# Kernel tuning notes

Hardware: AMD Instinct MI355X
Metric: run time of the kernel (lower is better)

Reference implementation:

```python
import jax, jax.numpy as jnp
import numpy as np

EPS = 1e-12  # torch F.normalize eps

def _l2norm(v, axis):
    n = jnp.linalg.norm(v, axis=axis, keepdims=True)
    return v / jnp.maximum(n, EPS)

def setup_inputs() -> dict:
    key = jax.random.key(0)
    k1, k2, k3 = jax.random.split(key, 3)
    N, D, H, W, K = 32, 512, 40, 40, 64
    x = jax.random.normal(k1, (N, D, H, W), dtype=jnp.float32)
    conv_weight = jax.random.normal(k2, (K, D), dtype=jnp.float32) * 0.05
    centroids = jax.random.uniform(k3, (K, D), dtype=jnp.float32)
    return {"x": x, "conv_weight": conv_weight, "centroids": centroids}

def reference(x, conv_weight, centroids):
    N, D, H, W = x.shape
    K = centroids.shape[0]
    # descriptor-wise L2 normalization over channel dim
    x = _l2norm(x, axis=1)
    x_flat = x.reshape(N, D, H * W)                       # [N, D, S]
    # 1x1 conv == per-pixel linear: [K,D] @ [N,D,S] -> [N,K,S]
    logits = jnp.einsum('kd,nds->nks', conv_weight, x_flat)
    soft_assign = jax.nn.softmax(logits, axis=1)          # softmax over clusters
    # vlad[n,k,d] = sum_s a[n,k,s] * (x[n,d,s] - c[k,d])
    #            = (a @ x^T) - (sum_s a) * c   -- two GEMM-like ops, no K-loop
    agg = jnp.einsum('nks,nds->nkd', soft_assign, x_flat)  # [N, K, D]
    a_sum = soft_assign.sum(axis=2)                        # [N, K]
    vlad = agg - a_sum[:, :, None] * centroids[None, :, :]
    # intra-normalization over D, flatten, global L2 normalization
    vlad = _l2norm(vlad, axis=2)
    vlad = vlad.reshape(N, K * D)
    vlad = _l2norm(vlad, axis=1)
    return vlad
```

## Files before the change

kernel.cpp:

```cpp
#include <hip/hip_runtime.h>
#include <math.h>

#define N_ 32
#define D_ 512
#define S_ 1600
#define K_ 64

typedef __attribute__((ext_vector_type(8))) short short8;
typedef __attribute__((ext_vector_type(4))) float f32x4;

static __device__ __forceinline__ short f2bf(float f) {
    unsigned u = __float_as_uint(f);
    u += 0x7fffu + ((u >> 16) & 1u);
    return (short)(u >> 16);
}

__global__ __launch_bounds__(256) void kW(const float* __restrict__ w,
                                          short* __restrict__ w16)
{
    int i4 = (blockIdx.x * 256 + threadIdx.x) * 4;
    float4 v = *(const float4*)&w[i4];
    short4 h = {f2bf(v.x), f2bf(v.y), f2bf(v.z), f2bf(v.w)};
    *(short4*)&w16[i4] = h;
}

#define TP 72

__global__ __launch_bounds__(256) void kA(const float* __restrict__ x,
                                          const short* __restrict__ w16,
                                          short* __restrict__ aprime,
                                          float* __restrict__ asum)
{
    __shared__ short T[64 * TP];
    __shared__ float pssq[16 * 66];
    __shared__ float invL[64];
    __shared__ float wred[2][4][64];

    const int tid = threadIdx.x;
    const int n  = blockIdx.x / 25;
    const int s0 = (blockIdx.x % 25) * 64;
    const int wv = tid >> 6;
    const int l  = tid & 63;
    const int lk = l & 15;
    const int q  = l >> 4;

    const float* xb = x + (size_t)n * D_ * S_ + s0;
    const int sg = (tid & 15) * 4;
    const int dg = tid >> 4;

    f32x4 acc[4];
#pragma unroll
    for (int st = 0; st < 4; ++st) acc[st] = (f32x4){0.f, 0.f, 0.f, 0.f};
    float ssql[4] = {0.f, 0.f, 0.f, 0.f};

    for (int dc = 0; dc < D_; dc += 64) {
        __syncthreads();
#pragma unroll
        for (int j = 0; j < 4; ++j) {
            int dci = dg + 16 * j;
            float4 v = *(const float4*)&xb[(size_t)(dc + dci) * S_ + sg];
            ssql[0] += v.x * v.x;  ssql[1] += v.y * v.y;
            ssql[2] += v.z * v.z;  ssql[3] += v.w * v.w;
            T[(sg + 0) * TP + dci] = f2bf(v.x);
            T[(sg + 1) * TP + dci] = f2bf(v.y);
            T[(sg + 2) * TP + dci] = f2bf(v.z);
            T[(sg + 3) * TP + dci] = f2bf(v.w);
        }
        __syncthreads();

#pragma unroll
        for (int kst = 0; kst < 2; ++kst) {
            short8 af = *(const short8*)&w16[(16 * wv + lk) * D_ + dc + kst * 32 + q * 8];
#pragma unroll
            for (int st = 0; st < 4; ++st) {
                short8 bf = *(const short8*)&T[(st * 16 + lk) * TP + kst * 32 + q * 8];
                acc[st] = __builtin_amdgcn_mfma_f32_16x16x32_bf16(af, bf, acc[st], 0, 0, 0);
            }
        }
    }

    __syncthreads();
#pragma unroll
    for (int i = 0; i < 4; ++i) pssq[dg * 66 + sg + i] = ssql[i];
    __syncthreads();
    if (tid < 64) {
        float ss = 0.f;
#pragma unroll
        for (int g = 0; g < 16; ++g) ss += pssq[g * 66 + tid];
        invL[tid] = 1.0f / fmaxf(sqrtf(ss), 1e-12f);
    }
    __syncthreads();

    float lg[4][4], invv[4];
#pragma unroll
    for (int st = 0; st < 4; ++st) {
        invv[st] = invL[st * 16 + lk];
#pragma unroll
        for (int r = 0; r < 4; ++r) lg[st][r] = acc[st][r] * invv[st];
    }
    float mx[4];
#pragma unroll
    for (int st = 0; st < 4; ++st) {
        float m = fmaxf(fmaxf(lg[st][0], lg[st][1]), fmaxf(lg[st][2], lg[st][3]));
        m = fmaxf(m, __shfl_xor(m, 16));
        m = fmaxf(m, __shfl_xor(m, 32));
        mx[st] = m;
        if (q == 0) wred[0][wv][st * 16 + lk] = m;
    }
    __syncthreads();
    float gm[4];
#pragma unroll
    for (int st = 0; st < 4; ++st) {
        float m = wred[0][0][st * 16 + lk];
        m = fmaxf(m, wred[0][1][st * 16 + lk]);
        m = fmaxf(m, wred[0][2][st * 16 + lk]);
        m = fmaxf(m, wred[0][3][st * 16 + lk]);
        gm[st] = m;
    }
    float e[4][4];
#pragma unroll
    for (int st = 0; st < 4; ++st) {
        float s = 0.f;
#pragma unroll
        for (int r = 0; r < 4; ++r) {
            e[st][r] = __expf(lg[st][r] - gm[st]);
            s += e[st][r];
        }
        s += __shfl_xor(s, 16);
        s += __shfl_xor(s, 32);
        if (q == 0) wred[1][wv][st * 16 + lk] = s;
    }
    __syncthreads();
    float rs[4];
#pragma unroll
    for (int st = 0; st < 4; ++st) {
        float s = wred[1][0][st * 16 + lk] + wred[1][1][st * 16 + lk]
                + wred[1][2][st * 16 + lk] + wred[1][3][st * 16 + lk];
        rs[st] = 1.0f / s;
    }

    short* apb = aprime + (size_t)n * K_ * S_ + s0;
#pragma unroll
    for (int r = 0; r < 4; ++r) {
        const int k = 16 * wv + 4 * q + r;
        float accp = 0.f;
#pragma unroll
        for (int st = 0; st < 4; ++st) {
            float p = e[st][r] * rs[st];
            apb[(size_t)k * S_ + st * 16 + lk] = f2bf(p * invv[st]);
            accp += p;
        }
        accp += __shfl_xor(accp, 1);
        accp += __shfl_xor(accp, 2);
        accp += __shfl_xor(accp, 4);
        accp += __shfl_xor(accp, 8);
        if (lk == 0) atomicAdd(&asum[n * K_ + k], accp);
    }
}

__global__ __launch_bounds__(256) void kB(const float* __restrict__ x,
                                          const short* __restrict__ aprime,
                                          float* __restrict__ aggp)
{
    const int bid = blockIdx.x;
    const int n  = bid / 20;
    const int dt = (bid % 20) / 5;
    const int sp = bid % 5;
    const int wv = threadIdx.x >> 6;
    const int l  = threadIdx.x & 63;
    const int lk = l & 15;
    const int q  = l >> 4;
    const int dbase = dt * 128 + wv * 32;

    const short* ap = aprime + (size_t)n * K_ * S_;
    const float* xb = x + (size_t)n * D_ * S_;

    f32x4 acc[4][2];
#pragma unroll
    for (int kt = 0; kt < 4; ++kt)
#pragma unroll
        for (int ds = 0; ds < 2; ++ds) acc[kt][ds] = (f32x4){0.f, 0.f, 0.f, 0.f};

    for (int kst = 0; kst < 10; ++kst) {
        const int s = sp * 320 + kst * 32 + q * 8;
        short8 af[4];
#pragma unroll
        for (int kt = 0; kt < 4; ++kt)
            af[kt] = *(const short8*)&ap[(size_t)(kt * 16 + lk) * S_ + s];
        short8 bf[2];
#pragma unroll
        for (int ds = 0; ds < 2; ++ds) {
            const float* xp = &xb[(size_t)(dbase + ds * 16 + lk) * S_ + s];
            float4 v0 = *(const float4*)xp;
            float4 v1 = *(const float4*)(xp + 4);
            short8 b;
            b[0] = f2bf(v0.x); b[1] = f2bf(v0.y); b[2] = f2bf(v0.z); b[3] = f2bf(v0.w);
            b[4] = f2bf(v1.x); b[5] = f2bf(v1.y); b[6] = f2bf(v1.z); b[7] = f2bf(v1.w);
            bf[ds] = b;
        }
#pragma unroll
        for (int kt = 0; kt < 4; ++kt)
#pragma unroll
            for (int ds = 0; ds < 2; ++ds)
                acc[kt][ds] = __builtin_amdgcn_mfma_f32_16x16x32_bf16(af[kt], bf[ds], acc[kt][ds], 0, 0, 0);
    }

    float* ab = aggp + ((size_t)sp * N_ + n) * K_ * D_;
#pragma unroll
    for (int kt = 0; kt < 4; ++kt)
#pragma unroll
        for (int ds = 0; ds < 2; ++ds)
#pragma unroll
            for (int r = 0; r < 4; ++r)
                ab[(size_t)(kt * 16 + 4 * q + r) * D_ + dbase + ds * 16 + lk] = acc[kt][ds][r];
}

__global__ __launch_bounds__(256) void kC(const float* __restrict__ aggp,
                                          const float* __restrict__ asum,
                                          const float* __restrict__ cent,
                                          float* __restrict__ out)
{
    __shared__ float red[4];
    const int tid = threadIdx.x;
    const int nk = blockIdx.x;
    const int k = nk & 63;
    const float as = asum[nk];
    const float* cb = cent + (size_t)k * D_;

    float v0 = 0.f, v1 = 0.f;
#pragma unroll
    for (int p = 0; p < 5; ++p) {
        const float* ag = aggp + (size_t)p * N_ * K_ * D_ + (size_t)nk * D_;
        v0 += ag[tid];
        v1 += ag[tid + 256];
    }
    v0 -= as * cb[tid];
    v1 -= as * cb[tid + 256];
    float ssq = v0 * v0 + v1 * v1;

    ssq += __shfl_xor(ssq, 32);
    ssq += __shfl_xor(ssq, 16);
    ssq += __shfl_xor(ssq, 8);
    ssq += __shfl_xor(ssq, 4);
    ssq += __shfl_xor(ssq, 2);
    ssq += __shfl_xor(ssq, 1);
    if ((tid & 63) == 0) red[tid >> 6] = ssq;
    __syncthreads();
    const float total = red[0] + red[1] + red[2] + red[3];
    const float scale = 1.0f / (fmaxf(sqrtf(total), 1e-12f) * 8.0f);

    out[(size_t)nk * D_ + tid]       = v0 * scale;
    out[(size_t)nk * D_ + tid + 256] = v1 * scale;
}

extern "C" void kernel_launch(void* const* d_in, const int* in_sizes, int n_in,
                              void* d_out, int out_size, void* d_ws, size_t ws_size,
                              hipStream_t stream)
{
    const float* x    = (const float*)d_in[0];
    const float* w    = (const float*)d_in[1];
    const float* cent = (const float*)d_in[2];
    float* out = (float*)d_out;

    float* aggp   = (float*)d_ws;
    float* asum   = aggp + (size_t)5 * N_ * K_ * D_;
    short* aprime = (short*)(asum + N_ * K_);
    short* w16    = aprime + (size_t)N_ * K_ * S_;

    hipMemsetAsync(asum, 0, (size_t)N_ * K_ * sizeof(float), stream);

    kW<<<32, 256, 0, stream>>>(w, w16);
    kA<<<N_ * (S_ / 64), 256, 0, stream>>>(x, w16, aprime, asum);
    kB<<<N_ * 4 * 5, 256, 0, stream>>>(x, aprime, aggp);
    kC<<<N_ * K_, 256, 0, stream>>>(aggp, asum, cent, out);
}
```

Baseline: 203.8 us.

## Fuse logits/softmax and aggregation kernels into one per-tile kernel

Merges the soft-assignment kernel and the aggregation GEMM into a single 512-thread kernel. Each block walks several 64-pixel tiles of one image, computes the normalized logits and softmax for the whole channel range, keeps the assignment tile in shared memory, and immediately accumulates it against x into register accumulators. This removes the bf16 assignment round trip through global memory and one launch. It also switches the x transpose to shuffle-based bf16 packing and changes the split-S partial count to 8. In exchange only 256 blocks run, each with heavy register and shared-memory use, and x is read twice within the block (once for the transpose, once for aggregation).

```diff
diff --git a/kernel.cpp b/kernel.cpp
--- a/kernel.cpp
+++ b/kernel.cpp
@@ -5,15 +5,24 @@
 #define D_ 512
 #define S_ 1600
 #define K_ 64
+#define NSP 8
+
+#define TP 536
+#define AP 72
+#define PP 68
 
 typedef __attribute__((ext_vector_type(8))) short short8;
 typedef __attribute__((ext_vector_type(4))) float f32x4;
+typedef __attribute__((ext_vector_type(2))) unsigned u32x2;
 
 static __device__ __forceinline__ short f2bf(float f) {
     unsigned u = __float_as_uint(f);
     u += 0x7fffu + ((u >> 16) & 1u);
     return (short)(u >> 16);
 }
+static __device__ __forceinline__ unsigned pk2(float a, float b) {
+    return (unsigned)(unsigned short)f2bf(a) | ((unsigned)(unsigned short)f2bf(b) << 16);
+}
 
 __global__ __launch_bounds__(256) void kW(const float* __restrict__ w,
                                           short* __restrict__ w16)
@@ -24,195 +33,176 @@
     *(short4*)&w16[i4] = h;
 }
 
-#define TP 72
-
-__global__ __launch_bounds__(256) void kA(const float* __restrict__ x,
-                                          const short* __restrict__ w16,
-                                          short* __restrict__ aprime,
-                                          float* __restrict__ asum)
+__global__ __launch_bounds__(512, 2) void kF(const float* __restrict__ x,
+                                             const short* __restrict__ w16,
+                                             float* __restrict__ aggp,
+                                             float* __restrict__ asum)
 {
     __shared__ short T[64 * TP];
-    __shared__ float pssq[16 * 66];
+    __shared__ short aP[64 * AP];
+    __shared__ float pssq[32 * PP];
     __shared__ float invL[64];
-    __shared__ float wred[2][4][64];
+    __shared__ float wredS[2][4][66];
 
     const int tid = threadIdx.x;
-    const int n  = blockIdx.x / 25;
-    const int s0 = (blockIdx.x % 25) * 64;
-    const int wv = tid >> 6;
-    const int l  = tid & 63;
-    const int lk = l & 15;
-    const int q  = l >> 4;
-
-    const float* xb = x + (size_t)n * D_ * S_ + s0;
-    const int sg = (tid & 15) * 4;
-    const int dg = tid >> 4;
-
-    f32x4 acc[4];
-#pragma unroll
-    for (int st = 0; st < 4; ++st) acc[st] = (f32x4){0.f, 0.f, 0.f, 0.f};
-    float ssql[4] = {0.f, 0.f, 0.f, 0.f};
-
-    for (int dc = 0; dc < D_; dc += 64) {
-        __syncthreads();
-#pragma unroll
-        for (int j = 0; j < 4; ++j) {
-            int dci = dg + 16 * j;
-            float4 v = *(const float4*)&xb[(size_t)(dc + dci) * S_ + sg];
+    const int wv  = tid >> 6;
+    const int l   = tid & 63;
+    const int lk  = l & 15;
+    const int q   = l >> 4;
+    const int kw  = wv & 3;
+    const int sgrp = wv >> 2;
+    const int dg  = tid >> 4;
+    const int n   = blockIdx.x >> 3;
+    const int bj  = blockIdx.x & 7;
+    const int nst = (bj == 0) ? 4 : 3;
+
+    const float* xb = x + (size_t)n * D_ * S_;
+
+    f32x4 acc[4][4];
+#pragma unroll
+    for (int a = 0; a < 4; ++a)
+#pragma unroll
+        for (int b = 0; b < 4; ++b) acc[a][b] = (f32x4){0.f, 0.f, 0.f, 0.f};
+    float asum_loc[4] = {0.f, 0.f, 0.f, 0.f};
+
+    for (int it = 0; it < nst; ++it) {
+        const int s0 = (bj + 8 * it) * 64;
+        __syncthreads();
+
+        float ssql[4] = {0.f, 0.f, 0.f, 0.f};
+#pragma unroll
+        for (int j = 0; j < 16; ++j) {
+            const int d = dg + 32 * j;
+            const float4 v = *(const float4*)&xb[(size_t)d * S_ + s0 + 4 * lk];
             ssql[0] += v.x * v.x;  ssql[1] += v.y * v.y;
             ssql[2] += v.z * v.z;  ssql[3] += v.w * v.w;
-            T[(sg + 0) * TP + dci] = f2bf(v.x);
-            T[(sg + 1) * TP + dci] = f2bf(v.y);
-            T[(sg + 2) * TP + dci] = f2bf(v.z);
-            T[(sg + 3) * TP + dci] = f2bf(v.w);
-        }
-        __syncthreads();
-
-#pragma unroll
-        for (int kst = 0; kst < 2; ++kst) {
-            short8 af = *(const short8*)&w16[(16 * wv + lk) * D_ + dc + kst * 32 + q * 8];
-#pragma unroll
-            for (int st = 0; st < 4; ++st) {
-                short8 bf = *(const short8*)&T[(st * 16 + lk) * TP + kst * 32 + q * 8];
-                acc[st] = __builtin_amdgcn_mfma_f32_16x16x32_bf16(af, bf, acc[st], 0, 0, 0);
+            unsigned p0 = pk2(v.x, v.y), p1 = pk2(v.z, v.w);
+            unsigned mine = (l & 32) ? p0 : p1;
+            unsigned oth  = (unsigned)__shfl_xor((int)mine, 32);
+            unsigned a0 = (l & 32) ? oth : p0;
+            unsigned a1 = (l & 32) ? p1 : oth;
+            unsigned r0 = (unsigned)__shfl_xor((int)a0, 16);
+            unsigned r1 = (unsigned)__shfl_xor((int)a1, 16);
+            unsigned o0, o1;
+            if (l & 16) {
+                o0 = (r0 >> 16) | (a0 & 0xffff0000u);
+                o1 = (r1 >> 16) | (a1 & 0xffff0000u);
+            } else {
+                o0 = (a0 & 0xffffu) | (r0 << 16);
+                o1 = (a1 & 0xffffu) | (r1 << 16);
             }
+            *(u32x2*)&T[(4 * lk + q) * TP + 4 * wv + 32 * j] = (u32x2){o0, o1};
+        }
+        *(float4*)&pssq[dg * PP + 4 * lk] = (float4){ssql[0], ssql[1], ssql[2], ssql[3]};
+        __syncthreads();
+
+        if (tid < 64) {
+            float ss = 0.f;
+#pragma unroll
+            for (int g = 0; g < 32; ++g) ss += pssq[g * PP + tid];
+            invL[tid] = 1.0f / fmaxf(sqrtf(ss), 1e-12f);
+        }
+
+        f32x4 accl0 = (f32x4){0.f, 0.f, 0.f, 0.f};
+        f32x4 accl1 = accl0;
+        const short* wrow = w16 + (size_t)(16 * kw + lk) * D_;
+        const short* tr0  = &T[(sgrp * 32 + lk) * TP];
+        const short* tr1  = tr0 + 16 * TP;
+#pragma unroll
+        for (int kst = 0; kst < 16; ++kst) {
+            short8 af = *(const short8*)&wrow[kst * 32 + q * 8];
+            short8 b0 = *(const short8*)&tr0[kst * 32 + q * 8];
+            short8 b1 = *(const short8*)&tr1[kst * 32 + q * 8];
+            accl0 = __builtin_amdgcn_mfma_f32_16x16x32_bf16(af, b0, accl0, 0, 0, 0);
+            accl1 = __builtin_amdgcn_mfma_f32_16x16x32_bf16(af, b1, accl1, 0, 0, 0);
+        }
+        __syncthreads();
+
+        const int sA0 = sgrp * 32 + lk;
+        const float invv0 = invL[sA0];
+        const float invv1 = invL[sA0 + 16];
+        float lg0[4], lg1[4];
+#pragma unroll
+        for (int r = 0; r < 4; ++r) { lg0[r] = accl0[r] * invv0; lg1[r] = accl1[r] * invv1; }
+        float m0 = fmaxf(fmaxf(lg0[0], lg0[1]), fmaxf(lg0[2], lg0[3]));
+        float m1 = fmaxf(fmaxf(lg1[0], lg1[1]), fmaxf(lg1[2], lg1[3]));
+        m0 = fmaxf(m0, __shfl_xor(m0, 16));  m0 = fmaxf(m0, __shfl_xor(m0, 32));
+        m1 = fmaxf(m1, __shfl_xor(m1, 16));  m1 = fmaxf(m1, __shfl_xor(m1, 32));
+        if (q == 0) { wredS[0][kw][sA0] = m0;  wredS[0][kw][sA0 + 16] = m1; }
+        __syncthreads();
+        const float gm0 = fmaxf(fmaxf(wredS[0][0][sA0], wredS[0][1][sA0]),
+                                fmaxf(wredS[0][2][sA0], wredS[0][3][sA0]));
+        const float gm1 = fmaxf(fmaxf(wredS[0][0][sA0 + 16], wredS[0][1][sA0 + 16]),
+                                fmaxf(wredS[0][2][sA0 + 16], wredS[0][3][sA0 + 16]));
+        float e0[4], e1[4];
+        float sm0 = 0.f, sm1 = 0.f;
+#pragma unroll
+        for (int r = 0; r < 4; ++r) {
+            e0[r] = __expf(lg0[r] - gm0);  sm0 += e0[r];
+            e1[r] = __expf(lg1[r] - gm1);  sm1 += e1[r];
+        }
+        sm0 += __shfl_xor(sm0, 16);  sm0 += __shfl_xor(sm0, 32);
+        sm1 += __shfl_xor(sm1, 16);  sm1 += __shfl_xor(sm1, 32);
+        if (q == 0) { wredS[1][kw][sA0] = sm0;  wredS[1][kw][sA0 + 16] = sm1; }
+        __syncthreads();
+        const float rs0 = 1.0f / (wredS[1][0][sA0] + wredS[1][1][sA0]
+                                + wredS[1][2][sA0] + wredS[1][3][sA0]);
+        const float rs1 = 1.0f / (wredS[1][0][sA0 + 16] + wredS[1][1][sA0 + 16]
+                                + wredS[1][2][sA0 + 16] + wredS[1][3][sA0 + 16]);
+#pragma unroll
+        for (int r = 0; r < 4; ++r) {
+            const int krow = 16 * kw + 4 * q + r;
+            const float pa = e0[r] * rs0;
+            const float pb = e1[r] * rs1;
+            aP[krow * AP + sA0]      = f2bf(pa * invv0);
+            aP[krow * AP + sA0 + 16] = f2bf(pb * invv1);
+            asum_loc[r] += pa + pb;
+        }
+        __syncthreads();
+
+        const int dbase = wv * 64;
+#pragma unroll
+        for (int k2 = 0; k2 < 2; ++k2) {
+            const int sA = k2 * 32 + q * 8;
+            short8 afr[4];
+#pragma unroll
+            for (int kt = 0; kt < 4; ++kt)
+                afr[kt] = *(const short8*)&aP[(kt * 16 + lk) * AP + sA];
+            short8 bfr[4];
+#pragma unroll
+            for (int ds = 0; ds < 4; ++ds) {
+                const float* xp = &xb[(size_t)(dbase + ds * 16 + lk) * S_ + s0 + sA];
+                float4 v0 = *(const float4*)xp;
+                float4 v1 = *(const float4*)(xp + 4);
+                short8 b;
+                b[0] = f2bf(v0.x); b[1] = f2bf(v0.y); b[2] = f2bf(v0.z); b[3] = f2bf(v0.w);
+                b[4] = f2bf(v1.x); b[5] = f2bf(v1.y); b[6] = f2bf(v1.z); b[7] = f2bf(v1.w);
+                bfr[ds] = b;
+            }
+#pragma unroll
+            for (int kt = 0; kt < 4; ++kt)
+#pragma unroll
+                for (int ds = 0; ds < 4; ++ds)
+                    acc[kt][ds] = __builtin_amdgcn_mfma_f32_16x16x32_bf16(afr[kt], bfr[ds], acc[kt][ds], 0, 0, 0);
         }
     }
 
-    __syncthreads();
-#pragma unroll
-    for (int i = 0; i < 4; ++i) pssq[dg * 66 + sg + i] = ssql[i];
-    __syncthreads();
-    if (tid < 64) {
-        float ss = 0.f;
-#pragma unroll
-        for (int g = 0; g < 16; ++g) ss += pssq[g * 66 + tid];
-        invL[tid] = 1.0f / fmaxf(sqrtf(ss), 1e-12f);
+    float* ab = aggp + ((size_t)bj * N_ + n) * K_ * D_;
+#pragma unroll
+    for (int kt = 0; kt < 4; ++kt)
+#pragma unroll
+        for (int ds = 0; ds < 4; ++ds)
+#pragma unroll
+            for (int r = 0; r < 4; ++r)
+                ab[(size_t)(kt * 16 + 4 * q + r) * D_ + wv * 64 + ds * 16 + lk] = acc[kt][ds][r];
+
+#pragma unroll
+    for (int r = 0; r < 4; ++r) {
+        float v = asum_loc[r];
+        v += __shfl_xor(v, 1);  v += __shfl_xor(v, 2);
+        v += __shfl_xor(v, 4);  v += __shfl_xor(v, 8);
+        if (lk == 0) atomicAdd(&asum[n * K_ + 16 * kw + 4 * q + r], v);
     }
-    __syncthreads();
-
-    float lg[4][4], invv[4];
-#pragma unroll
-    for (int st = 0; st < 4; ++st) {
-        invv[st] = invL[st * 16 + lk];
-#pragma unroll
-        for (int r = 0; r < 4; ++r) lg[st][r] = acc[st][r] * invv[st];
-    }
-    float mx[4];
-#pragma unroll
-    for (int st = 0; st < 4; ++st) {
-        float m = fmaxf(fmaxf(lg[st][0], lg[st][1]), fmaxf(lg[st][2], lg[st][3]));
-        m = fmaxf(m, __shfl_xor(m, 16));
-        m = fmaxf(m, __shfl_xor(m, 32));
-        mx[st] = m;
-        if (q == 0) wred[0][wv][st * 16 + lk] = m;
-    }
-    __syncthreads();
-    float gm[4];
-#pragma unroll
-    for (int st = 0; st < 4; ++st) {
-        float m = wred[0][0][st * 16 + lk];
-        m = fmaxf(m, wred[0][1][st * 16 + lk]);
-        m = fmaxf(m, wred[0][2][st * 16 + lk]);
-        m = fmaxf(m, wred[0][3][st * 16 + lk]);
-        gm[st] = m;
-    }
-    float e[4][4];
-#pragma unroll
-    for (int st = 0; st < 4; ++st) {
-        float s = 0.f;
-#pragma unroll
-        for (int r = 0; r < 4; ++r) {
-            e[st][r] = __expf(lg[st][r] - gm[st]);
-            s += e[st][r];
-        }
-        s += __shfl_xor(s, 16);
-        s += __shfl_xor(s, 32);
-        if (q == 0) wred[1][wv][st * 16 + lk] = s;
-    }
-    __syncthreads();
-    float rs[4];
-#pragma unroll
-    for (int st = 0; st < 4; ++st) {
-        float s = wred[1][0][st * 16 + lk] + wred[1][1][st * 16 + lk]
-                + wred[1][2][st * 16 + lk] + wred[1][3][st * 16 + lk];
-        rs[st] = 1.0f / s;
-    }
-
-    short* apb = aprime + (size_t)n * K_ * S_ + s0;
-#pragma unroll
-    for (int r = 0; r < 4; ++r) {
-        const int k = 16 * wv + 4 * q + r;
-        float accp = 0.f;
-#pragma unroll
-        for (int st = 0; st < 4; ++st) {
-            float p = e[st][r] * rs[st];
-            apb[(size_t)k * S_ + st * 16 + lk] = f2bf(p * invv[st]);
-            accp += p;
-        }
-        accp += __shfl_xor(accp, 1);
-        accp += __shfl_xor(accp, 2);
-        accp += __shfl_xor(accp, 4);
-        accp += __shfl_xor(accp, 8);
-        if (lk == 0) atomicAdd(&asum[n * K_ + k], accp);
-    }
-}
-
-__global__ __launch_bounds__(256) void kB(const float* __restrict__ x,
-                                          const short* __restrict__ aprime,
-                                          float* __restrict__ aggp)
-{
-    const int bid = blockIdx.x;
-    const int n  = bid / 20;
-    const int dt = (bid % 20) / 5;
-    const int sp = bid % 5;
-    const int wv = threadIdx.x >> 6;
-    const int l  = threadIdx.x & 63;
-    const int lk = l & 15;
-    const int q  = l >> 4;
-    const int dbase = dt * 128 + wv * 32;
-
-    const short* ap = aprime + (size_t)n * K_ * S_;
-    const float* xb = x + (size_t)n * D_ * S_;
-
-    f32x4 acc[4][2];
-#pragma unroll
-    for (int kt = 0; kt < 4; ++kt)
-#pragma unroll
-        for (int ds = 0; ds < 2; ++ds) acc[kt][ds] = (f32x4){0.f, 0.f, 0.f, 0.f};
-
-    for (int kst = 0; kst < 10; ++kst) {
-        const int s = sp * 320 + kst * 32 + q * 8;
-        short8 af[4];
-#pragma unroll
-        for (int kt = 0; kt < 4; ++kt)
-            af[kt] = *(const short8*)&ap[(size_t)(kt * 16 + lk) * S_ + s];
-        short8 bf[2];
-#pragma unroll
-        for (int ds = 0; ds < 2; ++ds) {
-            const float* xp = &xb[(size_t)(dbase + ds * 16 + lk) * S_ + s];
-            float4 v0 = *(const float4*)xp;
-            float4 v1 = *(const float4*)(xp + 4);
-            short8 b;
-            b[0] = f2bf(v0.x); b[1] = f2bf(v0.y); b[2] = f2bf(v0.z); b[3] = f2bf(v0.w);
-            b[4] = f2bf(v1.x); b[5] = f2bf(v1.y); b[6] = f2bf(v1.z); b[7] = f2bf(v1.w);
-            bf[ds] = b;
-        }
-#pragma unroll
-        for (int kt = 0; kt < 4; ++kt)
-#pragma unroll
-            for (int ds = 0; ds < 2; ++ds)
-                acc[kt][ds] = __builtin_amdgcn_mfma_f32_16x16x32_bf16(af[kt], bf[ds], acc[kt][ds], 0, 0, 0);
-    }
-
-    float* ab = aggp + ((size_t)sp * N_ + n) * K_ * D_;
-#pragma unroll
-    for (int kt = 0; kt < 4; ++kt)
-#pragma unroll
-        for (int ds = 0; ds < 2; ++ds)
-#pragma unroll
-            for (int r = 0; r < 4; ++r)
-                ab[(size_t)(kt * 16 + 4 * q + r) * D_ + dbase + ds * 16 + lk] = acc[kt][ds][r];
 }
 
 __global__ __launch_bounds__(256) void kC(const float* __restrict__ aggp,
@@ -229,7 +219,7 @@
 
     float v0 = 0.f, v1 = 0.f;
 #pragma unroll
-    for (int p = 0; p < 5; ++p) {
+    for (int p = 0; p < NSP; ++p) {
         const float* ag = aggp + (size_t)p * N_ * K_ * D_ + (size_t)nk * D_;
         v0 += ag[tid];
         v1 += ag[tid + 256];
@@ -262,15 +252,13 @@
     const float* cent = (const float*)d_in[2];
     float* out = (float*)d_out;
 
-    float* aggp   = (float*)d_ws;
-    float* asum   = aggp + (size_t)5 * N_ * K_ * D_;
-    short* aprime = (short*)(asum + N_ * K_);
-    short* w16    = aprime + (size_t)N_ * K_ * S_;
+    float* aggp = (float*)d_ws;
+    float* asum = aggp + (size_t)NSP * N_ * K_ * D_;
+    short* w16  = (short*)(asum + N_ * K_);
 
     hipMemsetAsync(asum, 0, (size_t)N_ * K_ * sizeof(float), stream);
 
     kW<<<32, 256, 0, stream>>>(w, w16);
-    kA<<<N_ * (S_ / 64), 256, 0, stream>>>(x, w16, aprime, asum);
-    kB<<<N_ * 4 * 5, 256, 0, stream>>>(x, aprime, aggp);
+    kF<<<N_ * NSP, 512, 0, stream>>>(x, w16, aggp, asum);
     kC<<<N_ * K_, 256, 0, stream>>>(aggp, asum, cent, out);
 }
```

After: 221.6 us. 1.09x slower.
